# Optimization experiments

Measured on AMD Instinct MI355X. Metric: run time of the kernel, lower is better.

## Reference

```python
import jax, jax.numpy as jnp
import numpy as np

EPS = 1e-12
NUM_KNOTS = 30


def _pchip_slopes(y, x):
    """Shape-preserving PCHIP slopes at knots. y,x: [K], K>2, x strictly increasing."""
    h = x[1:] - x[:-1]                      # [K-1]
    delta = (y[1:] - y[:-1]) / (h + EPS)    # [K-1]
    hkm1, hk = h[:-1], h[1:]
    w1 = 2.0 * hk + hkm1
    w2 = hk + 2.0 * hkm1
    same_sign = delta[:-1] * delta[1:] > 0
    d_int = (w1 + w2) / (w1 / (delta[:-1] + EPS) + w2 / (delta[1:] + EPS))
    d_mid = jnp.where(same_sign, d_int, jnp.zeros_like(d_int))  # [K-2]
    # one-sided endpoint slopes with monotonicity limiting
    d0 = ((2.0 * h[0] + h[1]) * delta[0] - h[0] * delta[1]) / (h[0] + h[1] + EPS)
    dN = ((2.0 * h[-1] + h[-2]) * delta[-1] - h[-1] * delta[-2]) / (h[-1] + h[-2] + EPS)

    def _limit(di, de):
        di = jnp.where(di * de <= 0, jnp.zeros_like(di), di)
        return jnp.where(jnp.abs(di) > 3.0 * jnp.abs(de), 3.0 * de, di)

    d0 = _limit(d0, delta[0])
    dN = _limit(dN, delta[-1])
    return jnp.concatenate([d0[None], d_mid, dN[None]])  # [K]


def setup_inputs() -> dict:
    key = jax.random.key(0)
    k1, k2 = jax.random.split(key)
    x = jax.random.uniform(k1, (8192, 4096), dtype=jnp.float32)  # inputs inside knot domain [0,1)
    knots = jnp.linspace(0.0, 1.0, NUM_KNOTS, dtype=jnp.float32)  # buffer: uniform knots
    coeffs = jax.random.normal(k2, (NUM_KNOTS,), dtype=jnp.float32) * 0.5  # learned knot values
    return {"x": x, "knots": knots, "coeffs": coeffs}


def reference(x, knots, coeffs):
    """PCHIP cubic Hermite spline evaluated elementwise at x."""
    K = knots.shape[0]
    d = _pchip_slopes(coeffs, knots)
    xc = jnp.clip(x, knots[0], knots[-1])
    idx = jnp.clip(jnp.searchsorted(knots, xc) - 1, 0, K - 2)
    xk, xk1 = knots[idx], knots[idx + 1]
    yk, yk1 = coeffs[idx], coeffs[idx + 1]
    dk, dk1 = d[idx], d[idx + 1]
    h = xk1 - xk
    safe_h = jnp.where(jnp.abs(h) < EPS, jnp.ones_like(h), h)
    t = jnp.where(jnp.abs(h) < EPS, jnp.zeros_like(xc), (xc - xk) / safe_h)
    t2 = t * t
    t3 = t2 * t
    h00 = 2.0 * t3 - 3.0 * t2 + 1.0
    h10 = t3 - 2.0 * t2 + t
    h01 = -2.0 * t3 + 3.0 * t2
    h11 = t3 - t2
    return h00 * yk + h10 * safe_h * dk + h01 * yk1 + h11 * safe_h * dk1
```

## Files before the change

kernel.cpp:

```cpp
#include <hip/hip_runtime.h>

#define EPSF 1e-12f
#define NKNOTS 30
#define NINT 29


__device__ __forceinline__ float eval1(float xc, const float4* __restrict__ tab) {
    xc = fminf(fmaxf(xc, 0.0f), 1.0f);
    float s = xc * 29.0f;
    int idx = (int)s;
    idx = idx > (NINT - 1) ? (NINT - 1) : idx;
    float t = s - (float)idx;
    float4 c = tab[idx];
    return fmaf(t, fmaf(t, fmaf(t, c.w, c.z), c.y), c.x);
}

__global__ __launch_bounds__(256) void SimpleSpline_kernel(
    const float* __restrict__ x,
    const float* __restrict__ knots,
    const float* __restrict__ coeffs,
    float* __restrict__ out,
    int n)
{
    __shared__ float4 tab[NINT];
    __shared__ float dsh[NKNOTS];

    const int tid = threadIdx.x;

    if (tid < NKNOTS) {
        float d;
        if (tid == 0) {
            float h0 = knots[1] - knots[0];
            float h1 = knots[2] - knots[1];
            float de0 = (coeffs[1] - coeffs[0]) / (h0 + EPSF);
            float de1 = (coeffs[2] - coeffs[1]) / (h1 + EPSF);
            d = ((2.0f * h0 + h1) * de0 - h0 * de1) / (h0 + h1 + EPSF);
            if (d * de0 <= 0.0f) d = 0.0f;
            if (fabsf(d) > 3.0f * fabsf(de0)) d = 3.0f * de0;
        } else if (tid == NKNOTS - 1) {
            float hN = knots[NKNOTS - 1] - knots[NKNOTS - 2];
            float hM = knots[NKNOTS - 2] - knots[NKNOTS - 3];
            float deN = (coeffs[NKNOTS - 1] - coeffs[NKNOTS - 2]) / (hN + EPSF);
            float deM = (coeffs[NKNOTS - 2] - coeffs[NKNOTS - 3]) / (hM + EPSF);
            d = ((2.0f * hN + hM) * deN - hN * deM) / (hN + hM + EPSF);
            if (d * deN <= 0.0f) d = 0.0f;
            if (fabsf(d) > 3.0f * fabsf(deN)) d = 3.0f * deN;
        } else {
            float hkm1 = knots[tid] - knots[tid - 1];
            float hk   = knots[tid + 1] - knots[tid];
            float dkm1 = (coeffs[tid] - coeffs[tid - 1]) / (hkm1 + EPSF);
            float dk   = (coeffs[tid + 1] - coeffs[tid]) / (hk + EPSF);
            float w1 = 2.0f * hk + hkm1;
            float w2 = hk + 2.0f * hkm1;
            d = 0.0f;
            if (dkm1 * dk > 0.0f)
                d = (w1 + w2) / (w1 / (dkm1 + EPSF) + w2 / (dk + EPSF));
        }
        dsh[tid] = d;
    }
    __syncthreads();

    if (tid < NINT) {
        float h = knots[tid + 1] - knots[tid];
        float safe_h = (fabsf(h) < EPSF) ? 1.0f : h;
        float yk  = coeffs[tid];
        float yk1 = coeffs[tid + 1];
        float sdk  = safe_h * dsh[tid];
        float sdk1 = safe_h * dsh[tid + 1];
        tab[tid] = make_float4(yk,
                               sdk,
                               3.0f * (yk1 - yk) - 2.0f * sdk - sdk1,
                               2.0f * (yk - yk1) + sdk + sdk1);
    }
    __syncthreads();

    const int n4 = n >> 2;
    const float4* __restrict__ xv = (const float4*)x;
    float4* __restrict__ ov = (float4*)out;

    const int stride = gridDim.x * blockDim.x;
    for (int i = blockIdx.x * blockDim.x + tid; i < n4; i += stride) {
        float4 v = xv[i];
        float4 r;
        r.x = eval1(v.x, tab);
        r.y = eval1(v.y, tab);
        r.z = eval1(v.z, tab);
        r.w = eval1(v.w, tab);
        ov[i] = r;
    }

    const int rem = n & 3;
    if (rem) {
        const int base = n4 << 2;
        const int gi = blockIdx.x * blockDim.x + tid;
        if (gi < rem) out[base + gi] = eval1(x[base + gi], tab);
    }
}

extern "C" void kernel_launch(void* const* d_in, const int* in_sizes, int n_in,
                              void* d_out, int out_size, void* d_ws, size_t ws_size,
                              hipStream_t stream) {
    const float* x      = (const float*)d_in[0];
    const float* knots  = (const float*)d_in[1];
    const float* coeffs = (const float*)d_in[2];
    float* out = (float*)d_out;
    const int n = in_sizes[0];

    const int block = 256;
    int n4 = n >> 2;
    int blocks = (n4 + block - 1) / block;
    if (blocks > 4096) blocks = 4096;
    if (blocks < 1) blocks = 1;

    SimpleSpline_kernel<<<blocks, block, 0, stream>>>(x, knots, coeffs, out, n);
}
```

Before: 234.3 us.

## Split coefficient table into SoA, unroll grid-stride loop 4x, use nontemporal stores

Changes the shared coefficient table from a float4 array to four separate float arrays, so each lookup becomes four scalar LDS reads instead of one 128-bit read. The grid-stride loop is unrolled four times, issuing four independent vector loads before any compute so more memory requests are in flight per thread. Output writes use nontemporal stores to avoid polluting cache with streaming data. The split table quadruples LDS instruction count per element, and the unrolling raises register pressure.

```diff
diff --git a/kernel.cpp b/kernel.cpp
--- a/kernel.cpp
+++ b/kernel.cpp
@@ -4,16 +4,8 @@
 #define NKNOTS 30
 #define NINT 29
 
+typedef float fvec4 __attribute__((ext_vector_type(4)));
 
-__device__ __forceinline__ float eval1(float xc, const float4* __restrict__ tab) {
-    xc = fminf(fmaxf(xc, 0.0f), 1.0f);
-    float s = xc * 29.0f;
-    int idx = (int)s;
-    idx = idx > (NINT - 1) ? (NINT - 1) : idx;
-    float t = s - (float)idx;
-    float4 c = tab[idx];
-    return fmaf(t, fmaf(t, fmaf(t, c.w, c.z), c.y), c.x);
-}
 
 __global__ __launch_bounds__(256) void SimpleSpline_kernel(
     const float* __restrict__ x,
@@ -22,7 +14,7 @@
     float* __restrict__ out,
     int n)
 {
-    __shared__ float4 tab[NINT];
+    __shared__ float a0[NINT], a1[NINT], a2[NINT], a3[NINT];
     __shared__ float dsh[NKNOTS];
 
     const int tid = threadIdx.x;
@@ -67,33 +59,62 @@
         float yk1 = coeffs[tid + 1];
         float sdk  = safe_h * dsh[tid];
         float sdk1 = safe_h * dsh[tid + 1];
-        tab[tid] = make_float4(yk,
-                               sdk,
-                               3.0f * (yk1 - yk) - 2.0f * sdk - sdk1,
-                               2.0f * (yk - yk1) + sdk + sdk1);
+        a0[tid] = yk;
+        a1[tid] = sdk;
+        a2[tid] = 3.0f * (yk1 - yk) - 2.0f * sdk - sdk1;
+        a3[tid] = 2.0f * (yk - yk1) + sdk + sdk1;
     }
     __syncthreads();
 
+    auto eval1 = [&](float xc) -> float {
+        xc = fminf(fmaxf(xc, 0.0f), 1.0f);
+        float s = xc * 29.0f;
+        int idx = (int)s;
+        idx = idx > (NINT - 1) ? (NINT - 1) : idx;
+        float t = s - (float)idx;
+        float c0 = a0[idx], c1 = a1[idx], c2 = a2[idx], c3 = a3[idx];
+        return fmaf(t, fmaf(t, fmaf(t, c3, c2), c1), c0);
+    };
+
+    auto eval4 = [&](fvec4 v) -> fvec4 {
+        fvec4 r;
+        r.x = eval1(v.x);
+        r.y = eval1(v.y);
+        r.z = eval1(v.z);
+        r.w = eval1(v.w);
+        return r;
+    };
+
     const int n4 = n >> 2;
-    const float4* __restrict__ xv = (const float4*)x;
-    float4* __restrict__ ov = (float4*)out;
+    const fvec4* __restrict__ xv = (const fvec4*)x;
+    fvec4* __restrict__ ov = (fvec4*)out;
 
-    const int stride = gridDim.x * blockDim.x;
-    for (int i = blockIdx.x * blockDim.x + tid; i < n4; i += stride) {
-        float4 v = xv[i];
-        float4 r;
-        r.x = eval1(v.x, tab);
-        r.y = eval1(v.y, tab);
-        r.z = eval1(v.z, tab);
-        r.w = eval1(v.w, tab);
-        ov[i] = r;
+    const int gs = gridDim.x * blockDim.x;
+    int i = blockIdx.x * blockDim.x + tid;
+
+    for (; i + 3 * gs < n4; i += 4 * gs) {
+        fvec4 v0 = xv[i];
+        fvec4 v1 = xv[i + gs];
+        fvec4 v2 = xv[i + 2 * gs];
+        fvec4 v3 = xv[i + 3 * gs];
+        fvec4 r0 = eval4(v0);
+        fvec4 r1 = eval4(v1);
+        fvec4 r2 = eval4(v2);
+        fvec4 r3 = eval4(v3);
+        __builtin_nontemporal_store(r0, &ov[i]);
+        __builtin_nontemporal_store(r1, &ov[i + gs]);
+        __builtin_nontemporal_store(r2, &ov[i + 2 * gs]);
+        __builtin_nontemporal_store(r3, &ov[i + 3 * gs]);
+    }
+    for (; i < n4; i += gs) {
+        __builtin_nontemporal_store(eval4(xv[i]), &ov[i]);
     }
 
     const int rem = n & 3;
     if (rem) {
         const int base = n4 << 2;
         const int gi = blockIdx.x * blockDim.x + tid;
-        if (gi < rem) out[base + gi] = eval1(x[base + gi], tab);
+        if (gi < rem) out[base + gi] = eval1(x[base + gi]);
     }
 }
 
```

Measured after the change: 244.1 us. 1.04x slower.
